# Kernel tuning notes

Hardware: AMD Instinct MI355X
Metric: run time of the kernel (lower is better)

The kernel has to match this reference:

```python
import math
import jax, jax.numpy as jnp
import numpy as np

LAMBDA_TV = 0.005
LAMBDA_WAV = 0.005
MAX_ITER = 15
LEVELS = 3
TV_ITERS = 5  # prox_tv called with num_iter=5 in forward
S2 = math.sqrt(2.0)


def _fft2c(x):
    # x: (B, 2, H, W) real/imag channels -> centered 2D FFT, same layout
    xc = x[:, 0] + 1j * x[:, 1]
    kc = jnp.fft.fftshift(
        jnp.fft.fft2(jnp.fft.ifftshift(xc, axes=(-2, -1)), norm='ortho'),
        axes=(-2, -1))
    return jnp.stack([kc.real, kc.imag], axis=1)


def _ifft2c(x):
    xc = x[:, 0] + 1j * x[:, 1]
    ic = jnp.fft.fftshift(
        jnp.fft.ifft2(jnp.fft.ifftshift(xc, axes=(-2, -1)), norm='ortho'),
        axes=(-2, -1))
    return jnp.stack([ic.real, ic.imag], axis=1)


def _grad(x):
    # x: (N, 1, H, W) -> forward differences, (N, 2, H, W); last row/col zero
    dx = jnp.pad(x[:, :, :, 1:] - x[:, :, :, :-1], ((0, 0), (0, 0), (0, 0), (0, 1)))
    dy = jnp.pad(x[:, :, 1:, :] - x[:, :, :-1, :], ((0, 0), (0, 0), (0, 1), (0, 0)))
    return jnp.concatenate([dx, dy], axis=1)


def _div(p):
    # adjoint of _grad with the exact boundary handling of the torch code
    px, py = p[:, 0:1], p[:, 1:2]
    div_x = jnp.concatenate(
        [px[:, :, :, 0:1], px[:, :, :, 1:-1] - px[:, :, :, :-2], -px[:, :, :, -2:-1]],
        axis=-1)
    div_y = jnp.concatenate(
        [py[:, :, 0:1, :], py[:, :, 1:-1, :] - py[:, :, :-2, :], -py[:, :, -2:-1, :]],
        axis=2)
    return div_x + div_y


def _prox_tv(x, lam):
    # Chambolle dual iteration, applied per channel (vectorized over B*C)
    B, C, H, W = x.shape
    xc = x.reshape(B * C, 1, H, W)
    tau = 0.25

    def body(p, _):
        g = _grad(xc - lam * _div(p))
        pn = p + tau * g
        nrm = jnp.sqrt(jnp.sum(pn * pn, axis=1, keepdims=True) + 1e-8)
        return pn / jnp.maximum(nrm, 1.0), None

    p0 = jnp.zeros((B * C, 2, H, W), x.dtype)
    p, _ = jax.lax.scan(body, p0, None, length=TV_ITERS)
    return (xc - lam * _div(p)).reshape(B, C, H, W)


def _dwt2(x):
    x_lo = (x[:, :, :, ::2] + x[:, :, :, 1::2]) / S2
    x_hi = (x[:, :, :, ::2] - x[:, :, :, 1::2]) / S2
    ll = (x_lo[:, :, ::2] + x_lo[:, :, 1::2]) / S2
    lh = (x_lo[:, :, ::2] - x_lo[:, :, 1::2]) / S2
    hl = (x_hi[:, :, ::2] + x_hi[:, :, 1::2]) / S2
    hh = (x_hi[:, :, ::2] - x_hi[:, :, 1::2]) / S2
    return ll, (lh, hl, hh)


def _interleave(even, odd, axis):
    s = jnp.stack([even, odd], axis=axis + 1)
    shp = list(even.shape)
    shp[axis] *= 2
    return s.reshape(shp)


def _idwt2(ll, lh, hl, hh):
    x_lo = _interleave((ll + lh) / S2, (ll - lh) / S2, axis=2)  # rows
    x_hi = _interleave((hl + hh) / S2, (hl - hh) / S2, axis=2)
    return _interleave((x_lo + x_hi) / S2, (x_lo - x_hi) / S2, axis=3)  # cols


def _soft(x, t):
    return jnp.sign(x) * jnp.maximum(jnp.abs(x) - t, 0.0)


def setup_inputs() -> dict:
    key = jax.random.key(0)
    k1, k2 = jax.random.split(key)
    B, H, W = 16, 320, 320
    y = jax.random.normal(k1, (B, 2, H, W), jnp.float32)
    mask = (jax.random.uniform(k2, (B, 1, H, W)) < 0.3).astype(jnp.float32)
    return {"y": y, "mask": mask}


def reference(y, mask):
    def step(carry, _):
        x, z, t = carry
        # projected gradient for data fidelity (step_size = 1.0)
        g = _ifft2c(mask * (mask * _fft2c(z) - y))
        z_step = z - g
        # TV prox
        x_tv = _prox_tv(z_step, LAMBDA_TV)
        # wavelet decomposition + soft-threshold of detail subbands
        cur = x_tv
        details = []
        for _lvl in range(LEVELS):
            cur, d = _dwt2(cur)
            details.append(tuple(_soft(c, LAMBDA_WAV) for c in d))
        x_new = cur
        for d in reversed(details):
            x_new = _idwt2(x_new, *d)
        # FISTA momentum
        t_new = (1.0 + jnp.sqrt(1.0 + 4.0 * t * t)) / 2.0
        z_new = x_new + (t - 1.0) / t_new * (x_new - x)
        return (x_new, z_new, t_new), None

    x0 = _ifft2c(y)
    (x, _, _), _ = jax.lax.scan(jax.checkpoint(step), (x0, x0, jnp.float32(1.0)),
                                None, length=MAX_ITER)
    return x
```

## Files before the change

### kernel.cpp

```cpp
#include <hip/hip_runtime.h>
#include <math.h>

constexpr int WID  = 320;
constexpr int HWc  = 320 * 320;
constexpr int NIMG = 16;
constexpr int NSL  = 32;
constexpr int NTOT = NIMG * 2 * HWc;
constexpr float LAM_TV  = 0.005f;
constexpr float LAM_WAV = 0.005f;

__device__ __forceinline__ float softt(float v) {
    float a = fmaxf(fabsf(v) - LAM_WAV, 0.f);
    return copysignf(a, v);
}

__device__ __forceinline__ float fast_rsq(float x) {
    float r;
    asm volatile("v_rsq_f32 %0, %1" : "=v"(r) : "v"(x));
    return r;
}

struct Tw { float tc, ts; float stc[6], sts[6]; };

__global__ void build_tw(float* tb) {
    const int lane = threadIdx.x;
#pragma unroll
    for (int g = 0; g < 2; g++) {
        const float sgn = g ? 1.f : -1.f;
        float* p = tb + g * 14 * 64;
        float ts, tc;
        __sincosf(sgn * 6.283185307179586f * (float)lane / 320.f, &ts, &tc);
        p[lane] = tc; p[64 + lane] = ts;
#pragma unroll
        for (int s = 0; s < 6; s++) {
            int h = 32 >> s;
            int j = lane & (h - 1);
            float ang = sgn * 3.14159265358979323f * (float)j / (float)h;
            float ss, cc;
            __sincosf(ang, &ss, &cc);
            p[(2 + s) * 64 + lane] = cc;
            p[(8 + s) * 64 + lane] = ss;
        }
    }
}

__device__ __forceinline__ Tw load_tw(const float* __restrict__ tb, int lane) {
    Tw tw;
    tw.tc = tb[lane];
    tw.ts = tb[64 + lane];
#pragma unroll
    for (int s = 0; s < 6; s++) {
        tw.stc[s] = tb[(2 + s) * 64 + lane];
        tw.sts[s] = tb[(8 + s) * 64 + lane];
    }
    return tw;
}

template<int SGN>
__device__ __forceinline__ void fft320_core(const float (&vr)[5], const float (&vi)[5],
                                            float (&Cr)[5], float (&Ci)[5],
                                            const Tw& tw, int lane) {
    const float cw1 = 0.30901699437494745f, sw1 = 0.9510565162951535f;
    const float cw2 = -0.8090169943749475f, sw2 = 0.5877852522924731f;
    const float cwt[5] = {1.f, cw1, cw2, cw2, cw1};
    const float swt[5] = {0.f, sw1, sw2, -sw2, -sw1};
    Cr[0] = vr[0] + vr[1] + vr[2] + vr[3] + vr[4];
    Ci[0] = vi[0] + vi[1] + vi[2] + vi[3] + vi[4];
#pragma unroll
    for (int k = 1; k < 5; k++) {
        float ar = vr[0], ai = vi[0];
#pragma unroll
        for (int m = 1; m < 5; m++) {
            int j = (m * k) % 5;
            float wr_ = cwt[j], wi_ = (float)SGN * swt[j];
            ar += vr[m] * wr_ - vi[m] * wi_;
            ai += vr[m] * wi_ + vi[m] * wr_;
        }
        Cr[k] = ar; Ci[k] = ai;
    }
    float twr = 1.f, twi = 0.f;
#pragma unroll
    for (int k = 1; k < 5; k++) {
        float nr = twr * tw.tc - twi * tw.ts;
        twi = twr * tw.ts + twi * tw.tc;
        twr = nr;
        float r = Cr[k] * twr - Ci[k] * twi;
        Ci[k]   = Cr[k] * twi + Ci[k] * twr;
        Cr[k]   = r;
    }
#pragma unroll
    for (int s = 0; s < 6; s++) {
        int h = 32 >> s;
        bool up = (lane & h) != 0;
#pragma unroll
        for (int k = 0; k < 5; k++) {
            float orr = __shfl_xor(Cr[k], h);
            float oii = __shfl_xor(Ci[k], h);
            if (up) {
                float dr = orr - Cr[k], di = oii - Ci[k];
                Cr[k] = dr * tw.stc[s] - di * tw.sts[s];
                Ci[k] = dr * tw.sts[s] + di * tw.stc[s];
            } else {
                Cr[k] += orr;
                Ci[k] += oii;
            }
        }
    }
}

template<int SGN, int EPI>
__global__ __launch_bounds__(256) void fft_row(const float* __restrict__ in,
                                               float* __restrict__ out,
                                               const float* __restrict__ aux1,
                                               float* __restrict__ out2,
                                               const float* __restrict__ twb) {
    const int lane = threadIdx.x & 63;
    const int wv   = threadIdx.x >> 6;
    const int L    = blockIdx.x * 4 + wv;
    const int img  = L / 320;
    const int l    = L - img * 320;
    const size_t ibase = (size_t)img * 2 * HWc;
    const float* pre = in + ibase + (size_t)l * WID;
    const float* pim = pre + HWc;
    const int k1 = (int)(__brev((unsigned)lane) >> 26);

    Tw tw = load_tw(twb, lane);

    float vr[5], vi[5];
    const float sgn_in = (lane & 1) ? -1.f : 1.f;
#pragma unroll
    for (int m = 0; m < 5; m++) {
        int n = lane + 64 * m;
        vr[m] = sgn_in * pre[n];
        vi[m] = sgn_in * pim[n];
    }
    float zr[5], zi[5];
    if (EPI == 2) {
#pragma unroll
        for (int k = 0; k < 5; k++) {
            int idxs = 5 * k1 + k + l * WID;
            zr[k] = aux1[ibase + idxs];
            zi[k] = aux1[ibase + HWc + idxs];
        }
    }

    float Cr[5], Ci[5];
    fft320_core<SGN>(vr, vi, Cr, Ci, tw, lane);

    float* qre = out + ibase + (size_t)l * WID;
    float* qim = qre + HWc;
    const float scale = 0.05590169943749474f;
#pragma unroll
    for (int k = 0; k < 5; k++) {
        int kout = 5 * k1 + k;
        float s2 = (kout & 1) ? -scale : scale;
        float re = s2 * Cr[k];
        float im = s2 * Ci[k];
        const int idxs = kout + l * WID;
        if (EPI == 2) {
            re = zr[k] - re;
            im = zi[k] - im;
        }
        qre[kout] = re;
        qim[kout] = im;
        if (EPI == 3) {
            out2[ibase + idxs]       = re;
            out2[ibase + HWc + idxs] = im;
        }
    }
}

constexpr int CB   = 8;
constexpr int CPAD = CB + 1;

template<int SGN>
__device__ __forceinline__ void fft_line_lds(float (*tile)[320][CPAD], int cl,
                                             int lane, const Tw& tw) {
    float vr[5], vi[5], Cr[5], Ci[5];
    const float sgn_in = (lane & 1) ? -1.f : 1.f;
#pragma unroll
    for (int m = 0; m < 5; m++) {
        int n = lane + 64 * m;
        vr[m] = sgn_in * tile[0][n][cl];
        vi[m] = sgn_in * tile[1][n][cl];
    }
    fft320_core<SGN>(vr, vi, Cr, Ci, tw, lane);
    const int k1 = (int)(__brev((unsigned)lane) >> 26);
    const float scale = 0.05590169943749474f;
#pragma unroll
    for (int k = 0; k < 5; k++) {
        int kout = 5 * k1 + k;
        float s2 = (kout & 1) ? -scale : scale;
        tile[0][kout][cl] = s2 * Cr[k];
        tile[1][kout][cl] = s2 * Ci[k];
    }
}

template<int MODE>
__global__ __launch_bounds__(512) void fft_col(const float* __restrict__ in,
                                               float* __restrict__ out,
                                               const float* __restrict__ y,
                                               const float* __restrict__ mask,
                                               const float* __restrict__ twb) {
    __shared__ float tile[2][320][CPAD];
    const int tid = threadIdx.x;
    const int bpi = WID / CB;
    const int img = blockIdx.x / bpi;
    const int c0  = (blockIdx.x - img * bpi) * CB;
    const size_t ibase = (size_t)img * 2 * HWc;
    constexpr int C4 = CB / 4;
    constexpr int NE = 320 * C4;

#pragma unroll
    for (int comp = 0; comp < 2; comp++) {
        const float* p = in + ibase + (size_t)comp * HWc + c0;
        for (int i = tid; i < NE; i += 512) {
            int row = i >> 1, cg = (i & 1) << 2;
            float4 v = *(const float4*)(p + row * WID + cg);
            float* t = &tile[comp][row][cg];
            t[0] = v.x; t[1] = v.y; t[2] = v.z; t[3] = v.w;
        }
    }
    __syncthreads();

    const int lane = tid & 63;
    const int wv   = tid >> 6;

    if (MODE == 1) {
        Tw twf = load_tw(twb, lane);
        fft_line_lds<-1>(tile, wv, lane, twf);
        __syncthreads();
        const float* pm  = mask + (size_t)img * HWc + c0;
        const float* pyr = y + ibase + c0;
        const float* pyi = y + ibase + HWc + c0;
        for (int i = tid; i < NE; i += 512) {
            int row = i >> 1, cg = (i & 1) << 2;
            float4 m4 = *(const float4*)(pm  + row * WID + cg);
            float4 yr = *(const float4*)(pyr + row * WID + cg);
            float4 yi = *(const float4*)(pyi + row * WID + cg);
            float* tr = &tile[0][row][cg];
            float* ti = &tile[1][row][cg];
            tr[0] = m4.x * (m4.x * tr[0] - yr.x);
            tr[1] = m4.y * (m4.y * tr[1] - yr.y);
            tr[2] = m4.z * (m4.z * tr[2] - yr.z);
            tr[3] = m4.w * (m4.w * tr[3] - yr.w);
            ti[0] = m4.x * (m4.x * ti[0] - yi.x);
            ti[1] = m4.y * (m4.y * ti[1] - yi.y);
            ti[2] = m4.z * (m4.z * ti[2] - yi.z);
            ti[3] = m4.w * (m4.w * ti[3] - yi.w);
        }
        __syncthreads();
    }
    {
        Tw twi = load_tw(twb + 14 * 64, lane);
        fft_line_lds<1>(tile, wv, lane, twi);
    }
    __syncthreads();
#pragma unroll
    for (int comp = 0; comp < 2; comp++) {
        float* p = out + ibase + (size_t)comp * HWc + c0;
        for (int i = tid; i < NE; i += 512) {
            int row = i >> 1, cg = (i & 1) << 2;
            const float* t = &tile[comp][row][cg];
            *(float4*)(p + row * WID + cg) = make_float4(t[0], t[1], t[2], t[3]);
        }
    }
}

constexpr int HALO = 4;
constexpr int TIR = 8;
constexpr int TVR = TIR + 2 * HALO;
constexpr int TIC = 48;
constexpr int TCOLS = 7;
constexpr int TROWS = WID / TIR;
constexpr int TPS = TROWS * TCOLS;
constexpr int NEDGE = 2 * TCOLS + 2 * (TROWS - 2);

template<bool EDGE>
__device__ __forceinline__ void tv_core(const float* __restrict__ g, int gi0, int gj,
                                        float (&uf)[TIR]) {
    float z_[TVR], px_[TVR], py_[TVR];
    const bool colin = !EDGE || ((unsigned)gj < (unsigned)WID);
#pragma unroll
    for (int r = 0; r < TVR; r++) {
        int gi = gi0 + r;
        float v = 0.f;
        if (!EDGE) {
            v = g[gi * WID + gj];
        } else {
            bool in = colin && ((unsigned)gi < (unsigned)WID);
            if (in) v = g[gi * WID + gj];
        }
        z_[r] = v; px_[r] = 0.f; py_[r] = 0.f;
    }
    const bool gj_le0 = EDGE && (gj <= 0);
    const bool gj_hi  = EDGE && (gj >= WID - 1);
    const bool gx_on  = !EDGE || (gj < WID - 1);

#pragma clang loop unroll(disable)
    for (int it = 0; it < 5; it++) {
        float u_[TVR], sh[TVR];
#pragma unroll
        for (int r = 0; r < TVR; r++) sh[r] = __shfl_up(px_[r], 1);
#pragma unroll
        for (int r = 0; r < TVR; r++) {
            float divx, divy;
            if (!EDGE) {
                divx = px_[r] - sh[r];
                divy = (r > 0) ? py_[r] - py_[r - 1] : 0.f;
            } else {
                int gi = gi0 + r;
                divx = gj_le0 ? px_[r] : (gj_hi ? -sh[r] : px_[r] - sh[r]);
                float pym = (r > 0) ? py_[r - 1] : py_[0];
                divy = (gi <= 0) ? py_[r]
                     : ((gi >= WID - 1) ? -pym : py_[r] - pym);
            }
            u_[r] = z_[r] - LAM_TV * (divx + divy);
        }
#pragma unroll
        for (int r = 0; r < TVR; r++) sh[r] = __shfl_down(u_[r], 1);
#pragma unroll
        for (int r = 0; r < TVR; r++) {
            float gx, gy;
            if (!EDGE) {
                gx = sh[r] - u_[r];
                gy = (r < TVR - 1) ? u_[r + 1] - u_[r] : 0.f;
            } else {
                int gi = gi0 + r;
                float ub = (r < TVR - 1) ? u_[r + 1] : u_[r];
                gx = gx_on ? sh[r] - u_[r] : 0.f;
                gy = (gi < WID - 1 && r < TVR - 1) ? ub - u_[r] : 0.f;
            }
            float px = fmaf(0.25f, gx, px_[r]);
            float py = fmaf(0.25f, gy, py_[r]);
            float n2 = fmaf(px, px, fmaf(py, py, 1e-8f));
            float inv = fminf(fast_rsq(n2), 1.f);
            px_[r] = px * inv;
            py_[r] = py * inv;
        }
    }
    float shf[TIR];
#pragma unroll
    for (int r = HALO; r < TVR - HALO; r++) shf[r - HALO] = __shfl_up(px_[r], 1);
#pragma unroll
    for (int r = HALO; r < TVR - HALO; r++) {
        float pxm = shf[r - HALO];
        float divx, divy;
        if (!EDGE) {
            divx = px_[r] - pxm;
            divy = py_[r] - py_[r - 1];
        } else {
            int gi = gi0 + r;
            divx = gj_le0 ? px_[r] : (gj_hi ? -pxm : px_[r] - pxm);
            divy = (gi <= 0) ? py_[r]
                 : ((gi >= WID - 1) ? -py_[r - 1] : py_[r] - py_[r - 1]);
        }
        uf[r - HALO] = z_[r] - LAM_TV * (divx + divy);
    }
}

template<bool STOREZ>
__global__ __launch_bounds__(256) void tv_wav_fista(const float* __restrict__ zs,
                                                    float* __restrict__ x,
                                                    float* __restrict__ z,
                                                    float beta) {
    const int lane = threadIdx.x & 63;
    const int wv   = __builtin_amdgcn_readfirstlane(threadIdx.x >> 6);
    const int w    = blockIdx.x * 4 + wv;
    const int sl   = w / TPS;
    const int rem  = w - sl * TPS;
    int trow, tcol;
    if (rem < 2 * TCOLS) {
        trow = (rem < TCOLS) ? 0 : (TROWS - 1);
        tcol = (rem < TCOLS) ? rem : rem - TCOLS;
    } else if (rem < NEDGE) {
        int e = rem - 2 * TCOLS;
        trow = 1 + (e % (TROWS - 2));
        tcol = (e < TROWS - 2) ? 0 : (TCOLS - 1);
    } else {
        int i2 = rem - NEDGE;
        trow = 1 + i2 / (TCOLS - 2);
        tcol = 1 + i2 % (TCOLS - 2);
    }
    const int gi0  = trow * TIR - HALO;
    const int gj   = tcol * TIC - 8 + lane;
    const float* g = zs + (size_t)sl * HWc;

    float uf[TIR];
    if (rem >= NEDGE) tv_core<false>(g, gi0, gj, uf);
    else              tv_core<true >(g, gi0, gj, uf);

    const float sc1 = (lane & 1) ? -1.f : 1.f;
    const float sc2 = (lane & 2) ? -1.f : 1.f;
    const float sc3 = (lane & 4) ? -1.f : 1.f;

    float ll1[4], lh1[4], hl1[4], hh1[4];
#pragma unroll
    for (int k = 0; k < 4; k++) {
        float a0 = uf[2 * k], a1 = uf[2 * k + 1];
        float n0 = __shfl_xor(a0, 1), n1 = __shfl_xor(a1, 1);
        float h0 = a0 + n0, d0 = sc1 * (a0 - n0);
        float h1 = a1 + n1, d1 = sc1 * (a1 - n1);
        ll1[k] = (h0 + h1) * 0.5f;
        lh1[k] = softt((h0 - h1) * 0.5f);
        hl1[k] = softt((d0 + d1) * 0.5f);
        hh1[k] = softt((d0 - d1) * 0.5f);
    }
    float ll2[2], lh2[2], hl2[2], hh2[2];
#pragma unroll
    for (int k = 0; k < 2; k++) {
        float a0 = ll1[2 * k], a1 = ll1[2 * k + 1];
        float n0 = __shfl_xor(a0, 2), n1 = __shfl_xor(a1, 2);
        float h0 = a0 + n0, d0 = sc2 * (a0 - n0);
        float h1 = a1 + n1, d1 = sc2 * (a1 - n1);
        ll2[k] = (h0 + h1) * 0.5f;
        lh2[k] = softt((h0 - h1) * 0.5f);
        hl2[k] = softt((d0 + d1) * 0.5f);
        hh2[k] = softt((d0 - d1) * 0.5f);
    }
    float ll3, lh3, hl3, hh3;
    {
        float a0 = ll2[0], a1 = ll2[1];
        float n0 = __shfl_xor(a0, 4), n1 = __shfl_xor(a1, 4);
        float h0 = a0 + n0, d0 = sc3 * (a0 - n0);
        float h1 = a1 + n1, d1 = sc3 * (a1 - n1);
        ll3 = (h0 + h1) * 0.5f;
        lh3 = softt((h0 - h1) * 0.5f);
        hl3 = softt((d0 + d1) * 0.5f);
        hh3 = softt((d0 - d1) * 0.5f);
    }
    float l2p[2];
    l2p[0] = 0.5f * ((ll3 + lh3) + sc3 * (hl3 + hh3));
    l2p[1] = 0.5f * ((ll3 - lh3) + sc3 * (hl3 - hh3));
    float l1p[4];
#pragma unroll
    for (int k = 0; k < 2; k++) {
        l1p[2 * k]     = 0.5f * ((l2p[k] + lh2[k]) + sc2 * (hl2[k] + hh2[k]));
        l1p[2 * k + 1] = 0.5f * ((l2p[k] - lh2[k]) + sc2 * (hl2[k] - hh2[k]));
    }
    float xn[TIR];
#pragma unroll
    for (int k = 0; k < 4; k++) {
        xn[2 * k]     = 0.5f * ((l1p[k] + lh1[k]) + sc1 * (hl1[k] + hh1[k]));
        xn[2 * k + 1] = 0.5f * ((l1p[k] - lh1[k]) + sc1 * (hl1[k] - hh1[k]));
    }

    const bool wcol = (lane >= 8) && (lane < 56) && ((unsigned)gj < (unsigned)WID);
    float* px = x + (size_t)sl * HWc;
    float* pz = z + (size_t)sl * HWc;
    const int gi_int0 = trow * TIR;
#pragma unroll
    for (int i = 0; i < TIR; i++) {
        int off = (gi_int0 + i) * WID + gj;
        if (STOREZ) {
            float xo = wcol ? px[off] : 0.f;
            float zn = xn[i] + beta * (xn[i] - xo);
            if (wcol) {
                px[off] = xn[i];
                pz[off] = zn;
            }
        } else {
            if (wcol) px[off] = xn[i];
        }
    }
}

extern "C" void kernel_launch(void* const* d_in, const int* in_sizes, int n_in,
                              void* d_out, int out_size, void* d_ws, size_t ws_size,
                              hipStream_t stream) {
    const float* y    = (const float*)d_in[0];
    const float* mask = (const float*)d_in[1];
    float* x = (float*)d_out;

    float* ws = (float*)d_ws;
    float* z  = ws;
    float* t1 = ws + (size_t)NTOT;
    float* t2 = ws + 2 * (size_t)NTOT;
    float* tw = ws + 3 * (size_t)NTOT;
    float* twF = tw;
    float* twI = tw + 14 * 64;

    const int ROW_BLKS = (NIMG * 320) / 4;
    const int COL_BLKS = NIMG * (WID / CB);
    const int TV_BLKS  = (NSL * TPS) / 4;

    build_tw<<<1, 64, 0, stream>>>(tw);

    fft_col<0><<<COL_BLKS, 512, 0, stream>>>(y, t1, nullptr, nullptr, twF);
    fft_row<1, 3><<<ROW_BLKS, 256, 0, stream>>>(t1, x, nullptr, z, twI);

    float t = 1.f;
    for (int it = 0; it < 15; it++) {
        fft_row<-1, 0><<<ROW_BLKS, 256, 0, stream>>>(z, t1, nullptr, nullptr, twF);
        fft_col<1><<<COL_BLKS, 512, 0, stream>>>(t1, t2, y, mask, twF);
        fft_row<1, 2><<<ROW_BLKS, 256, 0, stream>>>(t2, t1, z, nullptr, twI);

        float tn   = (1.f + sqrtf(1.f + 4.f * t * t)) * 0.5f;
        float beta = (t - 1.f) / tn;
        t = tn;
        if (it < 14)
            tv_wav_fista<true ><<<TV_BLKS, 256, 0, stream>>>(t1, x, z, beta);
        else
            tv_wav_fista<false><<<TV_BLKS, 256, 0, stream>>>(t1, x, z, beta);
    }
    (void)in_sizes; (void)n_in; (void)out_size; (void)ws_size;
}
```

Measured before the change: 1.244 ms.

## Share TV row halos across waves via LDS instead of redundant per-wave halos

Each 256-thread block now processes a 32-row strip cooperatively. The four waves own contiguous 8-row slabs, and only the top and bottom waves carry the 4-row outer halo. Neighbouring boundary values of py and u are exchanged through shared memory with __syncthreads each Chambolle iteration. This removes the redundant 4+4 halo-row computation and loads that every 8-row wave tile used to carry. In exchange it adds block-wide barriers inside the iteration loop and load imbalance between the 12-row and 8-row waves.

```diff
diff --git a/kernel.cpp b/kernel.cpp
--- a/kernel.cpp
+++ b/kernel.cpp
@@ -267,69 +267,111 @@
     }
 }
 
-constexpr int HALO = 4;
 constexpr int TIR = 8;
-constexpr int TVR = TIR + 2 * HALO;
 constexpr int TIC = 48;
-constexpr int TCOLS = 7;
-constexpr int TROWS = WID / TIR;
-constexpr int TPS = TROWS * TCOLS;
-constexpr int NEDGE = 2 * TCOLS + 2 * (TROWS - 2);
+constexpr int MR  = 12;
+constexpr int BRI = 32;
+constexpr int BROWSB = WID / BRI;
+constexpr int BCOLSB = 7;
+constexpr int BPS = BROWSB * BCOLSB;
+constexpr int NEDGEB = 2 * BCOLSB + 2 * (BROWSB - 2);
 
 template<bool EDGE>
-__device__ __forceinline__ void tv_core(const float* __restrict__ g, int gi0, int gj,
-                                        float (&uf)[TIR]) {
-    float z_[TVR], px_[TVR], py_[TVR];
+__device__ __forceinline__ void tv_core_cw(const float* __restrict__ g,
+        int gi0, int gj, int wv, bool nr12, bool hasUp, bool hasDn, bool w0,
+        float (*xpy)[64], float (*xub)[64], int lane, float (&uf)[TIR]) {
+    float z_[MR], px_[MR], py_[MR];
     const bool colin = !EDGE || ((unsigned)gj < (unsigned)WID);
 #pragma unroll
-    for (int r = 0; r < TVR; r++) {
+    for (int r = 0; r < MR; r++) { z_[r] = 0.f; px_[r] = 0.f; py_[r] = 0.f; }
+#pragma unroll
+    for (int r = 0; r < TIR; r++) {
         int gi = gi0 + r;
-        float v = 0.f;
-        if (!EDGE) {
-            v = g[gi * WID + gj];
-        } else {
-            bool in = colin && ((unsigned)gi < (unsigned)WID);
-            if (in) v = g[gi * WID + gj];
-        }
-        z_[r] = v; px_[r] = 0.f; py_[r] = 0.f;
+        if (!EDGE) z_[r] = g[gi * WID + gj];
+        else if (colin && ((unsigned)gi < (unsigned)WID)) z_[r] = g[gi * WID + gj];
+    }
+    if (nr12) {
+#pragma unroll
+        for (int r = TIR; r < MR; r++) {
+            int gi = gi0 + r;
+            if (!EDGE) z_[r] = g[gi * WID + gj];
+            else if (colin && ((unsigned)gi < (unsigned)WID)) z_[r] = g[gi * WID + gj];
+        }
     }
     const bool gj_le0 = EDGE && (gj <= 0);
     const bool gj_hi  = EDGE && (gj >= WID - 1);
     const bool gx_on  = !EDGE || (gj < WID - 1);
+    const int  wup    = (wv > 0) ? wv - 1 : 0;
+    const int  wdn    = (wv < 3) ? wv + 1 : 3;
 
 #pragma clang loop unroll(disable)
     for (int it = 0; it < 5; it++) {
-        float u_[TVR], sh[TVR];
-#pragma unroll
-        for (int r = 0; r < TVR; r++) sh[r] = __shfl_up(px_[r], 1);
-#pragma unroll
-        for (int r = 0; r < TVR; r++) {
+        float u_[MR], sh[MR];
+        xpy[wv][lane] = nr12 ? py_[MR - 1] : py_[TIR - 1];
+        __syncthreads();
+        const float pym_in = hasUp ? xpy[wup][lane] : 0.f;
+#pragma unroll
+        for (int r = 0; r < TIR; r++) sh[r] = __shfl_up(px_[r], 1);
+        if (nr12) {
+#pragma unroll
+            for (int r = TIR; r < MR; r++) sh[r] = __shfl_up(px_[r], 1);
+        }
+#pragma unroll
+        for (int r = 0; r < TIR; r++) {
             float divx, divy;
             if (!EDGE) {
                 divx = px_[r] - sh[r];
-                divy = (r > 0) ? py_[r] - py_[r - 1] : 0.f;
+                divy = (r > 0) ? py_[r] - py_[r - 1]
+                               : (hasUp ? py_[0] - pym_in : 0.f);
             } else {
                 int gi = gi0 + r;
                 divx = gj_le0 ? px_[r] : (gj_hi ? -sh[r] : px_[r] - sh[r]);
-                float pym = (r > 0) ? py_[r - 1] : py_[0];
+                float pym = (r > 0) ? py_[r - 1] : (hasUp ? pym_in : py_[0]);
                 divy = (gi <= 0) ? py_[r]
                      : ((gi >= WID - 1) ? -pym : py_[r] - pym);
             }
             u_[r] = z_[r] - LAM_TV * (divx + divy);
         }
-#pragma unroll
-        for (int r = 0; r < TVR; r++) sh[r] = __shfl_down(u_[r], 1);
-#pragma unroll
-        for (int r = 0; r < TVR; r++) {
+        if (nr12) {
+#pragma unroll
+            for (int r = TIR; r < MR; r++) {
+                float divx, divy;
+                if (!EDGE) {
+                    divx = px_[r] - sh[r];
+                    divy = py_[r] - py_[r - 1];
+                } else {
+                    int gi = gi0 + r;
+                    divx = gj_le0 ? px_[r] : (gj_hi ? -sh[r] : px_[r] - sh[r]);
+                    float pym = py_[r - 1];
+                    divy = (gi <= 0) ? py_[r]
+                         : ((gi >= WID - 1) ? -pym : py_[r] - pym);
+                }
+                u_[r] = z_[r] - LAM_TV * (divx + divy);
+            }
+        } else {
+#pragma unroll
+            for (int r = TIR; r < MR; r++) u_[r] = 0.f;
+        }
+        xub[wv][lane] = u_[0];
+        __syncthreads();
+        const float ub_in = hasDn ? xub[wdn][lane] : 0.f;
+#pragma unroll
+        for (int r = 0; r < TIR; r++) sh[r] = __shfl_down(u_[r], 1);
+        if (nr12) {
+#pragma unroll
+            for (int r = TIR; r < MR; r++) sh[r] = __shfl_down(u_[r], 1);
+        }
+#pragma unroll
+        for (int r = 0; r < TIR; r++) {
+            float ub = (r < TIR - 1) ? u_[r + 1] : (nr12 ? u_[TIR] : ub_in);
             float gx, gy;
             if (!EDGE) {
                 gx = sh[r] - u_[r];
-                gy = (r < TVR - 1) ? u_[r + 1] - u_[r] : 0.f;
+                gy = ub - u_[r];
             } else {
                 int gi = gi0 + r;
-                float ub = (r < TVR - 1) ? u_[r + 1] : u_[r];
                 gx = gx_on ? sh[r] - u_[r] : 0.f;
-                gy = (gi < WID - 1 && r < TVR - 1) ? ub - u_[r] : 0.f;
+                gy = (gi < WID - 1) ? ub - u_[r] : 0.f;
             }
             float px = fmaf(0.25f, gx, px_[r]);
             float py = fmaf(0.25f, gy, py_[r]);
@@ -338,25 +380,78 @@
             px_[r] = px * inv;
             py_[r] = py * inv;
         }
-    }
-    float shf[TIR];
-#pragma unroll
-    for (int r = HALO; r < TVR - HALO; r++) shf[r - HALO] = __shfl_up(px_[r], 1);
-#pragma unroll
-    for (int r = HALO; r < TVR - HALO; r++) {
-        float pxm = shf[r - HALO];
+        if (nr12) {
+#pragma unroll
+            for (int r = TIR; r < MR; r++) {
+                bool vb = (r < MR - 1) || hasDn;
+                float ub = (r < MR - 1) ? u_[r + 1] : ub_in;
+                float gx, gy;
+                if (!EDGE) {
+                    gx = sh[r] - u_[r];
+                    gy = vb ? ub - u_[r] : 0.f;
+                } else {
+                    int gi = gi0 + r;
+                    gx = gx_on ? sh[r] - u_[r] : 0.f;
+                    gy = (gi < WID - 1 && vb) ? ub - u_[r] : 0.f;
+                }
+                float px = fmaf(0.25f, gx, px_[r]);
+                float py = fmaf(0.25f, gy, py_[r]);
+                float n2 = fmaf(px, px, fmaf(py, py, 1e-8f));
+                float inv = fminf(fast_rsq(n2), 1.f);
+                px_[r] = px * inv;
+                py_[r] = py * inv;
+            }
+        }
+    }
+    xpy[wv][lane] = nr12 ? py_[MR - 1] : py_[TIR - 1];
+    __syncthreads();
+    const float pym_in = hasUp ? xpy[wup][lane] : 0.f;
+    float shf[MR], uff[MR];
+#pragma unroll
+    for (int r = 0; r < TIR; r++) shf[r] = __shfl_up(px_[r], 1);
+    if (w0) {
+#pragma unroll
+        for (int r = TIR; r < MR; r++) shf[r] = __shfl_up(px_[r], 1);
+    }
+#pragma unroll
+    for (int r = 0; r < TIR; r++) {
+        float pxm = shf[r];
+        float pyab = (r > 0) ? py_[r - 1] : pym_in;
         float divx, divy;
         if (!EDGE) {
             divx = px_[r] - pxm;
-            divy = py_[r] - py_[r - 1];
+            divy = py_[r] - pyab;
         } else {
             int gi = gi0 + r;
             divx = gj_le0 ? px_[r] : (gj_hi ? -pxm : px_[r] - pxm);
             divy = (gi <= 0) ? py_[r]
-                 : ((gi >= WID - 1) ? -py_[r - 1] : py_[r] - py_[r - 1]);
-        }
-        uf[r - HALO] = z_[r] - LAM_TV * (divx + divy);
-    }
+                 : ((gi >= WID - 1) ? -pyab : py_[r] - pyab);
+        }
+        uff[r] = z_[r] - LAM_TV * (divx + divy);
+    }
+    if (w0) {
+#pragma unroll
+        for (int r = TIR; r < MR; r++) {
+            float pxm = shf[r];
+            float pyab = py_[r - 1];
+            float divx, divy;
+            if (!EDGE) {
+                divx = px_[r] - pxm;
+                divy = py_[r] - pyab;
+            } else {
+                int gi = gi0 + r;
+                divx = gj_le0 ? px_[r] : (gj_hi ? -pxm : px_[r] - pxm);
+                divy = (gi <= 0) ? py_[r]
+                     : ((gi >= WID - 1) ? -pyab : py_[r] - pyab);
+            }
+            uff[r] = z_[r] - LAM_TV * (divx + divy);
+        }
+    } else {
+#pragma unroll
+        for (int r = TIR; r < MR; r++) uff[r] = 0.f;
+    }
+#pragma unroll
+    for (int i = 0; i < TIR; i++) uf[i] = w0 ? uff[i + 4] : uff[i];
 }
 
 template<bool STOREZ>
@@ -364,31 +459,42 @@
                                                     float* __restrict__ x,
                                                     float* __restrict__ z,
                                                     float beta) {
+    __shared__ float xpy[4][64];
+    __shared__ float xub[4][64];
     const int lane = threadIdx.x & 63;
     const int wv   = __builtin_amdgcn_readfirstlane(threadIdx.x >> 6);
-    const int w    = blockIdx.x * 4 + wv;
-    const int sl   = w / TPS;
-    const int rem  = w - sl * TPS;
-    int trow, tcol;
-    if (rem < 2 * TCOLS) {
-        trow = (rem < TCOLS) ? 0 : (TROWS - 1);
-        tcol = (rem < TCOLS) ? rem : rem - TCOLS;
-    } else if (rem < NEDGE) {
-        int e = rem - 2 * TCOLS;
-        trow = 1 + (e % (TROWS - 2));
-        tcol = (e < TROWS - 2) ? 0 : (TCOLS - 1);
+    const int b    = blockIdx.x;
+    const int sl   = b / BPS;
+    const int rem  = b - sl * BPS;
+    int brow, bcol;
+    if (rem < 2 * BCOLSB) {
+        brow = (rem < BCOLSB) ? 0 : (BROWSB - 1);
+        bcol = (rem < BCOLSB) ? rem : rem - BCOLSB;
+    } else if (rem < NEDGEB) {
+        int e = rem - 2 * BCOLSB;
+        brow = 1 + (e & 7);
+        bcol = (e < 8) ? 0 : (BCOLSB - 1);
     } else {
-        int i2 = rem - NEDGE;
-        trow = 1 + i2 / (TCOLS - 2);
-        tcol = 1 + i2 % (TCOLS - 2);
-    }
-    const int gi0  = trow * TIR - HALO;
-    const int gj   = tcol * TIC - 8 + lane;
+        int i2 = rem - NEDGEB;
+        brow = 1 + i2 / 5;
+        bcol = 1 + i2 - 5 * (i2 / 5);
+    }
+    const int base = brow * BRI;
+    const int gj   = bcol * TIC - 8 + lane;
+    const bool nr12  = (wv == 0) || (wv == 3);
+    const bool hasUp = (wv != 0);
+    const bool hasDn = (wv != 3);
+    const bool w0    = (wv == 0);
+    const int gi0  = base - 4 + ((wv == 0) ? 0 : 4 + 8 * wv);
     const float* g = zs + (size_t)sl * HWc;
+    const bool edge = (brow == 0) || (brow == BROWSB - 1) ||
+                      (bcol == 0) || (bcol == BCOLSB - 1);
 
     float uf[TIR];
-    if (rem >= NEDGE) tv_core<false>(g, gi0, gj, uf);
-    else              tv_core<true >(g, gi0, gj, uf);
+    if (!edge) tv_core_cw<false>(g, gi0, gj, wv, nr12, hasUp, hasDn, w0,
+                                 xpy, xub, lane, uf);
+    else       tv_core_cw<true >(g, gi0, gj, wv, nr12, hasUp, hasDn, w0,
+                                 xpy, xub, lane, uf);
 
     const float sc1 = (lane & 1) ? -1.f : 1.f;
     const float sc2 = (lane & 2) ? -1.f : 1.f;
@@ -448,7 +554,7 @@
     const bool wcol = (lane >= 8) && (lane < 56) && ((unsigned)gj < (unsigned)WID);
     float* px = x + (size_t)sl * HWc;
     float* pz = z + (size_t)sl * HWc;
-    const int gi_int0 = trow * TIR;
+    const int gi_int0 = base + 8 * wv;
 #pragma unroll
     for (int i = 0; i < TIR; i++) {
         int off = (gi_int0 + i) * WID + gj;
@@ -482,7 +588,7 @@
 
     const int ROW_BLKS = (NIMG * 320) / 4;
     const int COL_BLKS = NIMG * (WID / CB);
-    const int TV_BLKS  = (NSL * TPS) / 4;
+    const int TV_BLKS  = NSL * BPS;
 
     build_tw<<<1, 64, 0, stream>>>(tw);
 
```

After: 1.255 ms. About the same (+0.9%).

## Share TV halo rows across six waves via LDS instead of per-wave recompute

Applied to the files above, without the earlier changes.

The TV/wavelet/FISTA kernel is restructured so each 384-thread block covers 32 interior rows with 6 waves of 8 rows each. The outer waves serve as the 8-row halo, and neighbouring waves exchange boundary py and u values through shared memory every Chambolle iteration. Before, each wave recomputed a 16-row window (8 interior rows plus 4-row halos on each side), so half of its TV work was redundant. The trade is two __syncthreads per iteration and two halo waves per block that only compute TV, which lowers redundancy from 2x to 1.5x.

```diff
diff --git a/kernel.cpp b/kernel.cpp
--- a/kernel.cpp
+++ b/kernel.cpp
@@ -267,69 +267,76 @@
     }
 }
 
-constexpr int HALO = 4;
 constexpr int TIR = 8;
-constexpr int TVR = TIR + 2 * HALO;
 constexpr int TIC = 48;
-constexpr int TCOLS = 7;
-constexpr int TROWS = WID / TIR;
-constexpr int TPS = TROWS * TCOLS;
-constexpr int NEDGE = 2 * TCOLS + 2 * (TROWS - 2);
+constexpr int NW  = 6;
+constexpr int BRI = 32;
+constexpr int BROWSB = WID / BRI;
+constexpr int BCOLSB = 7;
+constexpr int BPS = BROWSB * BCOLSB;
+constexpr int NEDGEB = 2 * BCOLSB + 2 * (BROWSB - 2);
 
 template<bool EDGE>
-__device__ __forceinline__ void tv_core(const float* __restrict__ g, int gi0, int gj,
-                                        float (&uf)[TIR]) {
-    float z_[TVR], px_[TVR], py_[TVR];
+__device__ __forceinline__ void tv_core6(const float* __restrict__ g,
+        int gi0, int gj, int wv, bool hasUp, bool hasDn, bool wantUf,
+        float (*xpy)[64], float (*xub)[64], int lane, float (&uf)[TIR]) {
+    float z_[TIR], px_[TIR], py_[TIR];
     const bool colin = !EDGE || ((unsigned)gj < (unsigned)WID);
 #pragma unroll
-    for (int r = 0; r < TVR; r++) {
+    for (int r = 0; r < TIR; r++) {
         int gi = gi0 + r;
         float v = 0.f;
-        if (!EDGE) {
-            v = g[gi * WID + gj];
-        } else {
-            bool in = colin && ((unsigned)gi < (unsigned)WID);
-            if (in) v = g[gi * WID + gj];
-        }
+        if (!EDGE) v = g[gi * WID + gj];
+        else if (colin && ((unsigned)gi < (unsigned)WID)) v = g[gi * WID + gj];
         z_[r] = v; px_[r] = 0.f; py_[r] = 0.f;
     }
     const bool gj_le0 = EDGE && (gj <= 0);
     const bool gj_hi  = EDGE && (gj >= WID - 1);
     const bool gx_on  = !EDGE || (gj < WID - 1);
+    const int  wup    = (wv > 0) ? wv - 1 : 0;
+    const int  wdn    = (wv < NW - 1) ? wv + 1 : NW - 1;
 
 #pragma clang loop unroll(disable)
     for (int it = 0; it < 5; it++) {
-        float u_[TVR], sh[TVR];
-#pragma unroll
-        for (int r = 0; r < TVR; r++) sh[r] = __shfl_up(px_[r], 1);
-#pragma unroll
-        for (int r = 0; r < TVR; r++) {
+        float u_[TIR], sh[TIR];
+        xpy[wv][lane] = py_[TIR - 1];
+        __syncthreads();
+        const float pym_in = hasUp ? xpy[wup][lane] : 0.f;
+#pragma unroll
+        for (int r = 0; r < TIR; r++) sh[r] = __shfl_up(px_[r], 1);
+#pragma unroll
+        for (int r = 0; r < TIR; r++) {
             float divx, divy;
             if (!EDGE) {
                 divx = px_[r] - sh[r];
-                divy = (r > 0) ? py_[r] - py_[r - 1] : 0.f;
+                divy = (r > 0) ? py_[r] - py_[r - 1]
+                               : (hasUp ? py_[0] - pym_in : 0.f);
             } else {
                 int gi = gi0 + r;
                 divx = gj_le0 ? px_[r] : (gj_hi ? -sh[r] : px_[r] - sh[r]);
-                float pym = (r > 0) ? py_[r - 1] : py_[0];
+                float pym = (r > 0) ? py_[r - 1] : (hasUp ? pym_in : py_[0]);
                 divy = (gi <= 0) ? py_[r]
                      : ((gi >= WID - 1) ? -pym : py_[r] - pym);
             }
             u_[r] = z_[r] - LAM_TV * (divx + divy);
         }
-#pragma unroll
-        for (int r = 0; r < TVR; r++) sh[r] = __shfl_down(u_[r], 1);
-#pragma unroll
-        for (int r = 0; r < TVR; r++) {
+        xub[wv][lane] = u_[0];
+        __syncthreads();
+        const float ub_in = hasDn ? xub[wdn][lane] : 0.f;
+#pragma unroll
+        for (int r = 0; r < TIR; r++) sh[r] = __shfl_down(u_[r], 1);
+#pragma unroll
+        for (int r = 0; r < TIR; r++) {
+            float ub = (r < TIR - 1) ? u_[r + 1] : ub_in;
+            bool vok = (r < TIR - 1) || hasDn;
             float gx, gy;
             if (!EDGE) {
                 gx = sh[r] - u_[r];
-                gy = (r < TVR - 1) ? u_[r + 1] - u_[r] : 0.f;
+                gy = vok ? ub - u_[r] : 0.f;
             } else {
                 int gi = gi0 + r;
-                float ub = (r < TVR - 1) ? u_[r + 1] : u_[r];
                 gx = gx_on ? sh[r] - u_[r] : 0.f;
-                gy = (gi < WID - 1 && r < TVR - 1) ? ub - u_[r] : 0.f;
+                gy = (gi < WID - 1 && vok) ? ub - u_[r] : 0.f;
             }
             float px = fmaf(0.25f, gx, px_[r]);
             float py = fmaf(0.25f, gy, py_[r]);
@@ -339,56 +346,74 @@
             py_[r] = py * inv;
         }
     }
-    float shf[TIR];
-#pragma unroll
-    for (int r = HALO; r < TVR - HALO; r++) shf[r - HALO] = __shfl_up(px_[r], 1);
-#pragma unroll
-    for (int r = HALO; r < TVR - HALO; r++) {
-        float pxm = shf[r - HALO];
-        float divx, divy;
-        if (!EDGE) {
-            divx = px_[r] - pxm;
-            divy = py_[r] - py_[r - 1];
-        } else {
-            int gi = gi0 + r;
-            divx = gj_le0 ? px_[r] : (gj_hi ? -pxm : px_[r] - pxm);
-            divy = (gi <= 0) ? py_[r]
-                 : ((gi >= WID - 1) ? -py_[r - 1] : py_[r] - py_[r - 1]);
-        }
-        uf[r - HALO] = z_[r] - LAM_TV * (divx + divy);
+    xpy[wv][lane] = py_[TIR - 1];
+    __syncthreads();
+    if (wantUf) {
+        const float pym_in = hasUp ? xpy[wup][lane] : 0.f;
+        float shf[TIR];
+#pragma unroll
+        for (int r = 0; r < TIR; r++) shf[r] = __shfl_up(px_[r], 1);
+#pragma unroll
+        for (int r = 0; r < TIR; r++) {
+            float pxm = shf[r];
+            float pyab = (r > 0) ? py_[r - 1] : pym_in;
+            float divx, divy;
+            if (!EDGE) {
+                divx = px_[r] - pxm;
+                divy = py_[r] - pyab;
+            } else {
+                int gi = gi0 + r;
+                divx = gj_le0 ? px_[r] : (gj_hi ? -pxm : px_[r] - pxm);
+                divy = (gi <= 0) ? py_[r]
+                     : ((gi >= WID - 1) ? -pyab : py_[r] - pyab);
+            }
+            uf[r] = z_[r] - LAM_TV * (divx + divy);
+        }
     }
 }
 
 template<bool STOREZ>
-__global__ __launch_bounds__(256) void tv_wav_fista(const float* __restrict__ zs,
-                                                    float* __restrict__ x,
-                                                    float* __restrict__ z,
-                                                    float beta) {
+__global__ __launch_bounds__(384, 6) void tv_wav_fista(const float* __restrict__ zs,
+                                                       float* __restrict__ x,
+                                                       float* __restrict__ z,
+                                                       float beta) {
+    __shared__ float xpy[NW][64];
+    __shared__ float xub[NW][64];
     const int lane = threadIdx.x & 63;
     const int wv   = __builtin_amdgcn_readfirstlane(threadIdx.x >> 6);
-    const int w    = blockIdx.x * 4 + wv;
-    const int sl   = w / TPS;
-    const int rem  = w - sl * TPS;
-    int trow, tcol;
-    if (rem < 2 * TCOLS) {
-        trow = (rem < TCOLS) ? 0 : (TROWS - 1);
-        tcol = (rem < TCOLS) ? rem : rem - TCOLS;
-    } else if (rem < NEDGE) {
-        int e = rem - 2 * TCOLS;
-        trow = 1 + (e % (TROWS - 2));
-        tcol = (e < TROWS - 2) ? 0 : (TCOLS - 1);
+    const int b    = blockIdx.x;
+    const int sl   = b / BPS;
+    const int rem  = b - sl * BPS;
+    int brow, bcol;
+    if (rem < 2 * BCOLSB) {
+        brow = (rem < BCOLSB) ? 0 : (BROWSB - 1);
+        bcol = (rem < BCOLSB) ? rem : rem - BCOLSB;
+    } else if (rem < NEDGEB) {
+        int e = rem - 2 * BCOLSB;
+        brow = 1 + (e & 7);
+        bcol = (e < 8) ? 0 : (BCOLSB - 1);
     } else {
-        int i2 = rem - NEDGE;
-        trow = 1 + i2 / (TCOLS - 2);
-        tcol = 1 + i2 % (TCOLS - 2);
-    }
-    const int gi0  = trow * TIR - HALO;
-    const int gj   = tcol * TIC - 8 + lane;
+        int i2 = rem - NEDGEB;
+        brow = 1 + i2 / 5;
+        bcol = 1 + i2 - 5 * (i2 / 5);
+    }
+    const int base = brow * BRI;
+    const int gj   = bcol * TIC - 8 + lane;
+    const int gi0    = base + 8 * wv - 8;
+    const bool hasUp = (wv != 0);
+    const bool hasDn = (wv != NW - 1);
+    const bool wantUf = (wv >= 1) && (wv <= 4);
     const float* g = zs + (size_t)sl * HWc;
+    const bool edge = (brow == 0) || (brow == BROWSB - 1) ||
+                      (bcol == 0) || (bcol == BCOLSB - 1);
 
     float uf[TIR];
-    if (rem >= NEDGE) tv_core<false>(g, gi0, gj, uf);
-    else              tv_core<true >(g, gi0, gj, uf);
+    if (!edge) tv_core6<false>(g, gi0, gj, wv, hasUp, hasDn, wantUf,
+                               xpy, xub, lane, uf);
+    else       tv_core6<true >(g, gi0, gj, wv, hasUp, hasDn, wantUf,
+                               xpy, xub, lane, uf);
+
+    if (!wantUf) return;
 
     const float sc1 = (lane & 1) ? -1.f : 1.f;
     const float sc2 = (lane & 2) ? -1.f : 1.f;
@@ -448,7 +473,7 @@
     const bool wcol = (lane >= 8) && (lane < 56) && ((unsigned)gj < (unsigned)WID);
     float* px = x + (size_t)sl * HWc;
     float* pz = z + (size_t)sl * HWc;
-    const int gi_int0 = trow * TIR;
+    const int gi_int0 = gi0;
 #pragma unroll
     for (int i = 0; i < TIR; i++) {
         int off = (gi_int0 + i) * WID + gj;
@@ -482,7 +507,7 @@
 
     const int ROW_BLKS = (NIMG * 320) / 4;
     const int COL_BLKS = NIMG * (WID / CB);
-    const int TV_BLKS  = (NSL * TPS) / 4;
+    const int TV_BLKS  = NSL * BPS;
 
     build_tw<<<1, 64, 0, stream>>>(tw);
 
@@ -499,9 +524,9 @@
         float beta = (t - 1.f) / tn;
         t = tn;
         if (it < 14)
-            tv_wav_fista<true ><<<TV_BLKS, 256, 0, stream>>>(t1, x, z, beta);
+            tv_wav_fista<true ><<<TV_BLKS, 384, 0, stream>>>(t1, x, z, beta);
         else
-            tv_wav_fista<false><<<TV_BLKS, 256, 0, stream>>>(t1, x, z, beta);
+            tv_wav_fista<false><<<TV_BLKS, 384, 0, stream>>>(t1, x, z, beta);
     }
     (void)in_sizes; (void)n_in; (void)out_size; (void)ws_size;
 }
```

Result: no change. 1.266 ms (+1.8%).
